# Kernel optimization log

Hardware: AMD Instinct MI355X
Metric: run time of the kernel (lower is better)

## Reference

```python
import jax, jax.numpy as jnp
import numpy as np

N = 20000      # nodes
E = 640000     # edges
FIN = 256
FQK = 256


def setup_inputs() -> dict:
    key = jax.random.key(0)
    kx, ks, kd, kw = jax.random.split(key, 4)
    x = jax.random.normal(kx, (N, FIN), dtype=jnp.float32)
    # src must be sorted (original scatter_softmax assumes grouped index);
    # force last element to N-1 so nbatches == N as in batch[-1]+1.
    src = jnp.sort(jax.random.randint(ks, (E,), 0, N))
    src = src.at[-1].set(N - 1)
    dest = jax.random.randint(kd, (E,), 0, N)
    ei = jnp.stack([src, dest]).astype(jnp.int64)
    # nn.Linear(Fin, 2*Fqk, bias=False) weight: [2*Fqk, Fin]
    bound = 1.0 / np.sqrt(FIN)
    W = jax.random.uniform(kw, (2 * FQK, FIN), dtype=jnp.float32,
                           minval=-bound, maxval=bound)
    return {"x": x, "ei": ei, "W": W}


def reference(x, ei, W):
    src, dest = ei[0], ei[1]
    n_nodes = x.shape[0]
    scaling = FQK ** -0.5
    qk = x @ W.T                      # [N, 2*Fqk]
    q, k = jnp.split(qk, 2, axis=-1)  # each [N, Fqk]
    q = q * scaling
    # per-edge dot product: (q[src] . k[dest])  -> [E]
    aw = jnp.einsum('ef,ef->e', q[src], k[dest])
    # scatter softmax over edges grouped by src node (raw exp, as original)
    ex = jnp.exp(aw)
    expsum = jax.ops.segment_sum(ex, src, num_segments=n_nodes)  # [N]
    return ex / expsum[src]
```

## Files before the change

kernel.cpp:

```cpp
#include <hip/hip_runtime.h>
#include <cmath>

#define FIN 256
#define FQK 256
#define SCALING 0.0625f
#define MAX_SEG 256
#define ASTRIDE 264

typedef _Float16 f16_t;
typedef f16_t f16x8 __attribute__((ext_vector_type(8)));
typedef f16_t f16x2 __attribute__((ext_vector_type(2)));
typedef float f32x4 __attribute__((ext_vector_type(4)));

__device__ __forceinline__ f16x8 cvt8h(float4 a, float4 b) {
    f16x8 r;
    r[0] = (f16_t)a.x; r[1] = (f16_t)a.y; r[2] = (f16_t)a.z; r[3] = (f16_t)a.w;
    r[4] = (f16_t)b.x; r[5] = (f16_t)b.y; r[6] = (f16_t)b.z; r[7] = (f16_t)b.w;
    return r;
}

__device__ __forceinline__ float fdot2f(f16x2 a, f16x2 b, float c) {
#if __has_builtin(__builtin_amdgcn_fdot2)
    return __builtin_amdgcn_fdot2(a, b, c, false);
#else
    return c + (float)a[0] * (float)b[0] + (float)a[1] * (float)b[1];
#endif
}

union H16 { uint4 u; f16x2 h[4]; };
__device__ __forceinline__ float dot16(uint4 ya, uint4 xa, float acc) {
    H16 A; A.u = ya;
    H16 X; X.u = xa;
#pragma unroll
    for (int i = 0; i < 4; ++i) acc = fdot2f(A.h[i], X.h[i], acc);
    return acc;
}

__global__ __launch_bounds__(256) void m_seg_kernel(const float* __restrict__ W,
                                                    f16_t* __restrict__ MbF,
                                                    const int* __restrict__ src,
                                                    int* __restrict__ seg, int N, int E) {
    const int b = blockIdx.x;
    if (b < FIN) {
        const int f = b;
        const int k = threadIdx.x;
        const float* __restrict__ Wq = W;
        const float* __restrict__ Wk = W + FQK * FIN;
        float acc = 0.f;
#pragma unroll 8
        for (int c = 0; c < FQK; ++c)
            acc += Wq[c * FIN + f] * Wk[c * FIN + k];
        const int ft  = f >> 4, m16 = f & 15;
        const int kcI = k >> 5, q = (k >> 3) & 3, e = k & 7;
        MbF[(size_t)(((kcI * 16 + ft) * 64 + q * 16 + m16) * 8 + e)] =
            (f16_t)(acc * SCALING);
    } else {
        const int n = (b - FIN) * 256 + threadIdx.x;
        if (n > N) return;
        int lo = 0, hi = E;
        while (lo < hi) {
            const int mid = (lo + hi) >> 1;
            if (src[mid] < n) lo = mid + 1; else hi = mid;
        }
        seg[n] = lo;
    }
}

__global__ __launch_bounds__(256) void gemm_y_kernel(const float* __restrict__ x,
                                                     const f16_t* __restrict__ MbF,
                                                     f16_t* __restrict__ y,
                                                     f16_t* __restrict__ xh, int N) {
    __shared__ f16_t sA[16 * ASTRIDE];

    const int t    = threadIdx.x;
    const int wv   = t >> 6;
    const int lane = t & 63;
    const int q    = lane >> 4;
    const int m16  = lane & 15;
    const int n0   = blockIdx.x * 16;
    const int f0   = wv * 64;

    {
        const int rsub = t >> 5;
        const int col  = (t & 31) * 8;
#pragma unroll
        for (int p = 0; p < 2; ++p) {
            const int r  = p * 8 + rsub;
            const int n  = n0 + r;
            const int nc = n < N ? n : N - 1;
            const float* __restrict__ xp = x + (size_t)nc * FIN + col;
            const float4 a = *(const float4*)(xp);
            const float4 b = *(const float4*)(xp + 4);
            const f16x8 v = cvt8h(a, b);
            *(f16x8*)&sA[r * ASTRIDE + col] = v;
            if (n < N) *(f16x8*)(xh + (size_t)n * FIN + col) = v;
        }
    }
    __syncthreads();

    f32x4 acc[4] = {};

#pragma unroll
    for (int kc = 0; kc < FIN; kc += 32) {
        const f16x8 af = *(const f16x8*)&sA[m16 * ASTRIDE + kc + q * 8];
        const f16_t* __restrict__ bp =
            MbF + (size_t)(((kc >> 5) * 16 + (f0 >> 4)) * 64 + lane) * 8;
#pragma unroll
        for (int ft = 0; ft < 4; ++ft) {
            union { uint4 u; f16x8 v; } bu;
            bu.u = *(const uint4*)(bp + ft * 512);
            acc[ft] = __builtin_amdgcn_mfma_f32_16x16x32_f16(af, bu.v, acc[ft], 0, 0, 0);
        }
    }

    __syncthreads();
#pragma unroll
    for (int ft = 0; ft < 4; ++ft)
#pragma unroll
        for (int r = 0; r < 4; ++r)
            sA[(q * 4 + r) * ASTRIDE + f0 + ft * 16 + m16] = (f16_t)acc[ft][r];
    __syncthreads();

    {
        const int row = t >> 4;
        const int c   = (t & 15) * 16;
        const int n   = n0 + row;
        if (n < N) {
            const uint4 v0 = *(const uint4*)&sA[row * ASTRIDE + c];
            const uint4 v1 = *(const uint4*)&sA[row * ASTRIDE + c + 8];
            *(uint4*)(y + (size_t)n * FIN + c)     = v0;
            *(uint4*)(y + (size_t)n * FIN + c + 8) = v1;
        }
    }
}

__global__ __launch_bounds__(256) void node_edge_kernel(const f16_t* __restrict__ xh,
                                                        const f16_t* __restrict__ y,
                                                        const int* __restrict__ dest,
                                                        const int* __restrict__ seg,
                                                        float* __restrict__ out,
                                                        int N, int E, int nwaves) {
    __shared__ float exlds[4][MAX_SEG];

    const int w    = threadIdx.x >> 6;
    const int lane = threadIdx.x & 63;
    const int g    = lane >> 3;
    const int j    = lane & 7;

#define DCLAMP(d) ((unsigned)(d) < (unsigned)N ? (d) : 0)

#define GISSUE(B0, B1, B2, B3, i, valid)                                       \
    if (valid) {                                                               \
        const int d_ = DCLAMP(dest[s0 + (i)]);                                 \
        const uint4* __restrict__ yr = (const uint4*)(y + (size_t)d_ * FIN) + j * 4; \
        B0 = yr[0]; B1 = yr[1]; B2 = yr[2]; B3 = yr[3];                        \
    }

#define CONSUME(B0, B1, B2, B3, idx, valid)                                    \
    if (valid) {                                                               \
        float a_ = 0.f;                                                        \
        a_ = dot16(B0, X0, a_);                                                \
        a_ = dot16(B1, X1, a_);                                                \
        a_ = dot16(B2, X2, a_);                                                \
        a_ = dot16(B3, X3, a_);                                                \
        a_ += __shfl_xor(a_, 1, 64);                                           \
        a_ += __shfl_xor(a_, 2, 64);                                           \
        a_ += __shfl_xor(a_, 4, 64);                                           \
        const float ex = __expf(a_);                                           \
        sum += ex;                                                             \
        if (j == 0 && (idx) < MAX_SEG) exlds[w][idx] = ex;                     \
    }

    for (int n = blockIdx.x * 4 + w; n < N; n += nwaves) {
        int s0 = seg[n], s1 = seg[n + 1];
        s0 = min(max(s0, 0), E);
        s1 = min(max(s1, 0), E);
        const int cnt = s1 - s0;
        if (cnt <= 0) continue;

        const uint4* __restrict__ xp = (const uint4*)(xh + (size_t)n * FIN + j * 32);
        const uint4 X0 = xp[0], X1 = xp[1], X2 = xp[2], X3 = xp[3];

        float sum = 0.f;
        const int nit = (cnt + 7) >> 3;

        uint4 A0, A1, A2, A3, B0, B1, B2, B3;
        bool vA = g < cnt;
        GISSUE(A0, A1, A2, A3, g, vA);

        for (int it = 0; it < nit; it += 2) {
            const int iB = (it + 1) * 8 + g;
            const bool vB = iB < cnt;
            GISSUE(B0, B1, B2, B3, iB, vB);
            CONSUME(A0, A1, A2, A3, it * 8 + g, vA);
            const int iA = (it + 2) * 8 + g;
            vA = iA < cnt;
            GISSUE(A0, A1, A2, A3, iA, vA);
            CONSUME(B0, B1, B2, B3, iB, vB);
        }

        sum += __shfl_xor(sum, 8, 64);
        sum += __shfl_xor(sum, 16, 64);
        sum += __shfl_xor(sum, 32, 64);
        const float inv = 1.0f / sum;

        const int lim = cnt < MAX_SEG ? cnt : MAX_SEG;
        for (int i = lane; i < lim; i += 64)
            out[s0 + i] = exlds[w][i] * inv;
    }

#undef GISSUE
#undef CONSUME
#undef DCLAMP
}

extern "C" void kernel_launch(void* const* d_in, const int* in_sizes, int n_in,
                              void* d_out, int out_size, void* d_ws, size_t ws_size,
                              hipStream_t stream) {
    const float* x  = (const float*)d_in[0];
    const int*   ei = (const int*)d_in[1];
    const float* W  = (const float*)d_in[2];
    float* out = (float*)d_out;

    const int N = in_sizes[0] / FIN;
    const int E = in_sizes[1] / 2;

    f16_t* MbF = (f16_t*)d_ws;
    f16_t* y   = MbF + (size_t)FIN * FIN;
    f16_t* xh  = y + (size_t)N * FIN;
    int*   seg = (int*)(xh + (size_t)N * FIN);

    const int segBlocks = (N + 256) / 256;
    m_seg_kernel<<<FIN + segBlocks, 256, 0, stream>>>(W, MbF, ei, seg, N, E);

    gemm_y_kernel<<<(N + 15) / 16, 256, 0, stream>>>(x, MbF, y, xh, N);

    const int neBlocks = 1024;
    node_edge_kernel<<<neBlocks, 256, 0, stream>>>(xh, y, ei + E, seg, out,
                                                   N, E, neBlocks * 4);
}
```

Baseline: 132.8 us.

## Split fused per-node edge softmax into edge-parallel dot kernel plus segment normalize

Replaces the per-node wave loop, which gathered y rows for each source node and normalized in LDS, with an edge-parallel kernel that gives each wave an equal span of edges. That kernel also gathers the source x row and writes the unnormalized exp to global memory. A separate kernel then sums each segment and rescales it. The aim is to remove load imbalance from variable segment sizes and the MAX_SEG cap, at the cost of an extra x-row gather per edge, an extra kernel launch, and a global round trip of the output.

```diff
diff --git a/kernel.cpp b/kernel.cpp
--- a/kernel.cpp
+++ b/kernel.cpp
@@ -4,7 +4,6 @@
 #define FIN 256
 #define FQK 256
 #define SCALING 0.0625f
-#define MAX_SEG 256
 #define ASTRIDE 264
 
 typedef _Float16 f16_t;
@@ -134,84 +133,90 @@
     }
 }
 
-__global__ __launch_bounds__(256) void node_edge_kernel(const f16_t* __restrict__ xh,
-                                                        const f16_t* __restrict__ y,
-                                                        const int* __restrict__ dest,
-                                                        const int* __restrict__ seg,
-                                                        float* __restrict__ out,
-                                                        int N, int E, int nwaves) {
-    __shared__ float exlds[4][MAX_SEG];
-
+__global__ __launch_bounds__(256) void edge_dot_kernel(const f16_t* __restrict__ xh,
+                                                       const f16_t* __restrict__ y,
+                                                       const int* __restrict__ src,
+                                                       const int* __restrict__ dest,
+                                                       float* __restrict__ out,
+                                                       int N, int E, int span) {
     const int w    = threadIdx.x >> 6;
     const int lane = threadIdx.x & 63;
     const int g    = lane >> 3;
     const int j    = lane & 7;
 
-#define DCLAMP(d) ((unsigned)(d) < (unsigned)N ? (d) : 0)
-
-#define GISSUE(B0, B1, B2, B3, i, valid)                                       \
+    const int base = (blockIdx.x * 4 + w) * span;
+    if (base >= E) return;
+    const int end = min(base + span, E);
+
+#define ECLAMP(d, L) ((unsigned)(d) < (unsigned)(L) ? (d) : 0)
+
+#define EISSUE(Y0, Y1, Y2, Y3, X0, X1, X2, X3, e, valid)                       \
     if (valid) {                                                               \
-        const int d_ = DCLAMP(dest[s0 + (i)]);                                 \
-        const uint4* __restrict__ yr = (const uint4*)(y + (size_t)d_ * FIN) + j * 4; \
-        B0 = yr[0]; B1 = yr[1]; B2 = yr[2]; B3 = yr[3];                        \
-    }
-
-#define CONSUME(B0, B1, B2, B3, idx, valid)                                    \
+        const int d_ = ECLAMP(dest[e], N);                                     \
+        const int s_ = ECLAMP(src[e], N);                                      \
+        const uint4* __restrict__ yr = (const uint4*)(y + (size_t)d_ * FIN) + j * 4;  \
+        const uint4* __restrict__ xr = (const uint4*)(xh + (size_t)s_ * FIN) + j * 4; \
+        Y0 = yr[0]; Y1 = yr[1]; Y2 = yr[2]; Y3 = yr[3];                        \
+        X0 = xr[0]; X1 = xr[1]; X2 = xr[2]; X3 = xr[3];                        \
+    }
+
+#define ECONSUME(Y0, Y1, Y2, Y3, X0, X1, X2, X3, e, valid)                     \
     if (valid) {                                                               \
         float a_ = 0.f;                                                        \
-        a_ = dot16(B0, X0, a_);                                                \
-        a_ = dot16(B1, X1, a_);                                                \
-        a_ = dot16(B2, X2, a_);                                                \
-        a_ = dot16(B3, X3, a_);                                                \
+        a_ = dot16(Y0, X0, a_);                                                \
+        a_ = dot16(Y1, X1, a_);                                                \
+        a_ = dot16(Y2, X2, a_);                                                \
+        a_ = dot16(Y3, X3, a_);                                                \
         a_ += __shfl_xor(a_, 1, 64);                                           \
         a_ += __shfl_xor(a_, 2, 64);                                           \
         a_ += __shfl_xor(a_, 4, 64);                                           \
-        const float ex = __expf(a_);                                           \
-        sum += ex;                                                             \
-        if (j == 0 && (idx) < MAX_SEG) exlds[w][idx] = ex;                     \
-    }
-
-    for (int n = blockIdx.x * 4 + w; n < N; n += nwaves) {
-        int s0 = seg[n], s1 = seg[n + 1];
-        s0 = min(max(s0, 0), E);
-        s1 = min(max(s1, 0), E);
-        const int cnt = s1 - s0;
-        if (cnt <= 0) continue;
-
-        const uint4* __restrict__ xp = (const uint4*)(xh + (size_t)n * FIN + j * 32);
-        const uint4 X0 = xp[0], X1 = xp[1], X2 = xp[2], X3 = xp[3];
-
-        float sum = 0.f;
-        const int nit = (cnt + 7) >> 3;
-
-        uint4 A0, A1, A2, A3, B0, B1, B2, B3;
-        bool vA = g < cnt;
-        GISSUE(A0, A1, A2, A3, g, vA);
-
-        for (int it = 0; it < nit; it += 2) {
-            const int iB = (it + 1) * 8 + g;
-            const bool vB = iB < cnt;
-            GISSUE(B0, B1, B2, B3, iB, vB);
-            CONSUME(A0, A1, A2, A3, it * 8 + g, vA);
-            const int iA = (it + 2) * 8 + g;
-            vA = iA < cnt;
-            GISSUE(A0, A1, A2, A3, iA, vA);
-            CONSUME(B0, B1, B2, B3, iB, vB);
-        }
-
-        sum += __shfl_xor(sum, 8, 64);
-        sum += __shfl_xor(sum, 16, 64);
-        sum += __shfl_xor(sum, 32, 64);
-        const float inv = 1.0f / sum;
-
-        const int lim = cnt < MAX_SEG ? cnt : MAX_SEG;
-        for (int i = lane; i < lim; i += 64)
-            out[s0 + i] = exlds[w][i] * inv;
-    }
-
-#undef GISSUE
-#undef CONSUME
-#undef DCLAMP
+        if (j == 0) out[e] = __expf(a_);                                       \
+    }
+
+    uint4 A0, A1, A2, A3, AX0, AX1, AX2, AX3;
+    uint4 B0, B1, B2, B3, BX0, BX1, BX2, BX3;
+
+    int  eA = base + g;
+    bool vA = eA < end;
+    EISSUE(A0, A1, A2, A3, AX0, AX1, AX2, AX3, eA, vA);
+
+    const int nit = (end - base + 7) >> 3;
+    for (int it = 0; it < nit; it += 2) {
+        const int eB = base + (it + 1) * 8 + g;
+        const bool vB = eB < end;
+        EISSUE(B0, B1, B2, B3, BX0, BX1, BX2, BX3, eB, vB);
+        ECONSUME(A0, A1, A2, A3, AX0, AX1, AX2, AX3, eA, vA);
+        eA = base + (it + 2) * 8 + g;
+        vA = eA < end;
+        EISSUE(A0, A1, A2, A3, AX0, AX1, AX2, AX3, eA, vA);
+        ECONSUME(B0, B1, B2, B3, BX0, BX1, BX2, BX3, eB, vB);
+    }
+
+#undef EISSUE
+#undef ECONSUME
+#undef ECLAMP
+}
+
+__global__ __launch_bounds__(256) void segnorm_kernel(float* __restrict__ out,
+                                                      const int* __restrict__ seg,
+                                                      int N, int E) {
+    const int n = blockIdx.x * 32 + (threadIdx.x >> 3);
+    const int j = threadIdx.x & 7;
+    if (n >= N) return;
+
+    int s0 = seg[n], s1 = seg[n + 1];
+    s0 = min(max(s0, 0), E);
+    s1 = min(max(s1, 0), E);
+    if (s1 <= s0) return;
+
+    float sum = 0.f;
+    for (int i = s0 + j; i < s1; i += 8) sum += out[i];
+    sum += __shfl_xor(sum, 1, 64);
+    sum += __shfl_xor(sum, 2, 64);
+    sum += __shfl_xor(sum, 4, 64);
+    const float inv = 1.0f / sum;
+
+    for (int i = s0 + j; i < s1; i += 8) out[i] *= inv;
 }
 
 extern "C" void kernel_launch(void* const* d_in, const int* in_sizes, int n_in,
@@ -236,6 +241,9 @@
     gemm_y_kernel<<<(N + 15) / 16, 256, 0, stream>>>(x, MbF, y, xh, N);
 
     const int neBlocks = 1024;
-    node_edge_kernel<<<neBlocks, 256, 0, stream>>>(xh, y, ei + E, seg, out,
-                                                   N, E, neBlocks * 4);
-}
+    const int nwaves   = neBlocks * 4;
+    const int span     = ((E + nwaves - 1) / nwaves + 7) & ~7;
+    edge_dot_kernel<<<neBlocks, 256, 0, stream>>>(xh, y, ei, ei + E, out, N, E, span);
+
+    segnorm_kernel<<<(N + 31) / 32, 256, 0, stream>>>(out, seg, N, E);
+}
```

Result: slower. 145.3 us (+9.4%).
